# Optimization experiments

Hardware: AMD Instinct MI355X
Metric: run time of the kernel (lower is better)

Reference implementation:

```python
import jax, jax.numpy as jnp
import numpy as np

H = 16
D_NOPE = 128
D_ROPE = 64
D_V = 128
ROPE_BASE = 10000.0
NEG = -1e9


def rotate_half(x):
    h = x.shape[-1] // 2
    return jnp.concatenate([-x[..., h:], x[..., :h]], axis=-1)


def rope_cos_sin(L, dtype=jnp.float32):
    inv_freq = 1.0 / (ROPE_BASE ** (jnp.arange(0, D_ROPE, 2, dtype=jnp.float32) / D_ROPE))
    t = jnp.arange(L, dtype=jnp.float32)
    freqs = jnp.outer(t, inv_freq)                      # (L, D_ROPE/2)
    emb = jnp.concatenate([freqs, freqs], axis=-1)      # (L, D_ROPE)
    return jnp.cos(emb)[None, None].astype(dtype), jnp.sin(emb)[None, None].astype(dtype)


def setup_inputs() -> dict:
    key = jax.random.key(0)
    ks = jax.random.split(key, 8)
    B, L, D = 1, 2048, 2048
    dq, dc = 1536, 512
    dqk = D_NOPE + D_ROPE
    s = 0.02
    hidden_states = jax.random.normal(ks[0], (B, L, D), jnp.float32)
    # causal additive mask, shape (B,1,L,L)
    causal = jnp.tril(jnp.ones((L, L), jnp.bool_))
    attention_mask = jnp.where(causal, 0.0, NEG).astype(jnp.float32)[None, None]
    return {
        "hidden_states": hidden_states,
        "attention_mask": attention_mask,
        "Wq_down": jax.random.normal(ks[1], (D, dq), jnp.float32) * s,
        "Wq_up": jax.random.normal(ks[2], (dq, H * dqk), jnp.float32) * s,
        "Wkv_down": jax.random.normal(ks[3], (D, dc), jnp.float32) * s,
        "Wk_up": jax.random.normal(ks[4], (dc, H * dqk), jnp.float32) * s,
        "Wv_up": jax.random.normal(ks[5], (dc, H * D_V), jnp.float32) * s,
        "Wo": jax.random.normal(ks[6], (H * D_V, D), jnp.float32) * s,
    }


def reference(hidden_states, attention_mask, Wq_down, Wq_up, Wkv_down, Wk_up, Wv_up, Wo):
    B, L, D = hidden_states.shape
    dqk = D_NOPE + D_ROPE
    scale = 1.0 / np.sqrt(dqk).astype(np.float32)

    # low-rank Q path
    q = (hidden_states @ Wq_down) @ Wq_up                       # (B,L,H*dqk)
    q = q.reshape(B, L, H, dqk).transpose(0, 2, 1, 3)           # (B,H,L,dqk)
    # low-rank KV path
    c_kv = hidden_states @ Wkv_down                             # (B,L,dc)
    k = (c_kv @ Wk_up).reshape(B, L, H, dqk).transpose(0, 2, 1, 3)
    v = (c_kv @ Wv_up).reshape(B, L, H, D_V).transpose(0, 2, 1, 3)

    q_nope, q_rope = q[..., :D_NOPE], q[..., D_NOPE:]
    k_nope, k_rope = k[..., :D_NOPE], k[..., D_NOPE:]
    cos, sin = rope_cos_sin(L, hidden_states.dtype)
    q_rope = q_rope * cos + rotate_half(q_rope) * sin
    k_rope = k_rope * cos + rotate_half(k_rope) * sin
    q = jnp.concatenate([q_nope, q_rope], axis=-1)
    k = jnp.concatenate([k_nope, k_rope], axis=-1)

    scores = jnp.einsum("bhqd,bhkd->bhqk", q, k) * scale + attention_mask
    weights = jax.nn.softmax(scores.astype(jnp.float32), axis=-1).astype(q.dtype)
    attn = jnp.einsum("bhqk,bhkd->bhqd", weights, v)            # (B,H,L,D_V)
    attn = attn.transpose(0, 2, 1, 3).reshape(B, L, H * D_V)
    return attn @ Wo
```

## Files before the change

### kernel.cpp

```cpp
#include <hip/hip_runtime.h>
#include <hip/hip_bf16.h>

using bf16 = __hip_bfloat16;
typedef __bf16 bf16x8v __attribute__((ext_vector_type(8)));
typedef float f32x4 __attribute__((ext_vector_type(4)));

static constexpr int SEQ = 2048;
static constexpr int DMODEL = 2048;
static constexpr int NHEADS = 16;
static constexpr int DQKC = 192;
static constexpr int DVC = 128;
static constexpr int DQC = 1536;
static constexpr int DCC = 512;
static constexpr int HQK = NHEADS * DQKC;
static constexpr int HV = NHEADS * DVC;
static constexpr int NKV = HQK + HV;
static constexpr int NDOWN = DQC + DCC;

typedef __attribute__((address_space(1))) const void* gas_ptr;
typedef __attribute__((address_space(3))) void* las_ptr;

__device__ __forceinline__ void g2l16(const void* g, void* l) {
  __builtin_amdgcn_global_load_lds((gas_ptr)g, (las_ptr)l, 16, 0, 0);
}

template <int BM, int BN>
__device__ __forceinline__ void gemm_core(
    const bf16* __restrict__ A, int lda,
    const bf16* __restrict__ Bt, int ldb,
    void* __restrict__ Cv, int ldc,
    int K, float alpha, int c_fp32, long tm, long tn, char* smem)
{
  constexpr int FM = BM / 32, FN = BN / 32;
  bf16* As = (bf16*)smem;
  char* Bsm = smem + BM * 64;
  bf16* Bs = (bf16*)Bsm;
  const int tid = threadIdx.x;
  const int w = tid >> 6, lane = tid & 63;
  const int wm = (w >> 1) * (BM / 2), wn = (w & 1) * (BN / 2);
  const int m0 = lane & 15, q8 = (lane >> 4) * 8;
  f32x4 acc[FM][FN] = {};
  for (int bk = 0; bk < K; bk += 32) {
#pragma unroll
    for (int i = 0; i < BM / 64; i++) {
      const int u = i * 256 + tid;
      g2l16(A + (tm + (u >> 2)) * (long)lda + bk + (u & 3) * 8, smem + u * 16);
    }
#pragma unroll
    for (int i = 0; i < BN / 64; i++) {
      const int u = i * 256 + tid;
      g2l16(Bt + (tn + (u >> 2)) * (long)ldb + bk + (u & 3) * 8, Bsm + u * 16);
    }
    __syncthreads();
    bf16x8v af[FM], bfv[FN];
#pragma unroll
    for (int i = 0; i < FM; i++)
      af[i] = *reinterpret_cast<const bf16x8v*>(&As[(wm + i * 16 + m0) * 32 + q8]);
#pragma unroll
    for (int i = 0; i < FN; i++)
      bfv[i] = *reinterpret_cast<const bf16x8v*>(&Bs[(wn + i * 16 + m0) * 32 + q8]);
#pragma unroll
    for (int mi = 0; mi < FM; mi++)
#pragma unroll
      for (int ni = 0; ni < FN; ni++)
        acc[mi][ni] = __builtin_amdgcn_mfma_f32_16x16x32_bf16(af[mi], bfv[ni], acc[mi][ni], 0, 0, 0);
    __syncthreads();
  }
  const int q4 = (lane >> 4) * 4;
  float* Cf = (float*)Cv;
  bf16* Cb = (bf16*)Cv;
#pragma unroll
  for (int mi = 0; mi < FM; mi++) {
#pragma unroll
    for (int r = 0; r < 4; r++) {
      const long row = tm + wm + mi * 16 + q4 + r;
#pragma unroll
      for (int ni = 0; ni < FN; ni++) {
        const long idx = row * ldc + tn + wn + ni * 16 + m0;
        const float v = acc[mi][ni][r] * alpha;
        if (c_fp32) Cf[idx] = v;
        else Cb[idx] = __float2bfloat16(v);
      }
    }
  }
}

__global__ __launch_bounds__(256) void gemm64(
    const bf16* __restrict__ A, int lda, const bf16* __restrict__ Bt, int ldb,
    void* __restrict__ Cv, int ldc, int K, float alpha, int c_fp32)
{
  __shared__ __align__(16) char smem[(64 + 128) * 64];
  gemm_core<64, 128>(A, lda, Bt, ldb, Cv, ldc, K, alpha, c_fp32,
                     (long)blockIdx.y * 64, (long)blockIdx.x * 128, smem);
}

__global__ __launch_bounds__(256) void gemm_dual(
    const bf16* __restrict__ A1, int lda1, const bf16* __restrict__ B1, int ldb1,
    void* __restrict__ C1, int ldc1, int K1, float alpha1, int nx1,
    const bf16* __restrict__ A2, int lda2, const bf16* __restrict__ B2, int ldb2,
    void* __restrict__ C2, int ldc2, int K2)
{
  __shared__ __align__(16) char smem[(128 + 128) * 64];
  if ((int)blockIdx.x < nx1)
    gemm_core<128, 128>(A1, lda1, B1, ldb1, C1, ldc1, K1, alpha1, 0,
                        (long)blockIdx.y * 128, (long)blockIdx.x * 128, smem);
  else
    gemm_core<128, 128>(A2, lda2, B2, ldb2, C2, ldc2, K2, 1.f, 0,
                        (long)blockIdx.y * 128, (long)((int)blockIdx.x - nx1) * 128, smem);
}

__device__ __forceinline__ void fa_stage(
    const bf16* __restrict__ kvf, const bf16* __restrict__ vT,
    char* smem, int kbase, int vbase, int key0, int h, int tid)
{
#pragma unroll
  for (int i = 0; i < 9; i++) {
    const int u = i * 256 + tid;
    const int key = u / 24;
    const int fg = (u - key * 24) ^ (key & 7);
    g2l16(kvf + (long)(key0 + key) * NKV + h * DQKC + fg * 8, smem + kbase + u * 16);
  }
#pragma unroll
  for (int i = 0; i < 8; i++) {
    const int u = i * 256 + tid;
    const int dv = u >> 4;
    const int kg = (u & 15) ^ (dv & 15);
    g2l16(vT + (long)(h * DVC + dv) * SEQ + key0 + kg * 8, smem + vbase + u * 16);
  }
}

__global__ __launch_bounds__(256) void flash_attn(
    const bf16* __restrict__ qf,
    const bf16* __restrict__ kvf,
    const bf16* __restrict__ vT,
    bf16* __restrict__ attn)
{
  __shared__ __align__(16) char smem[155648];
  const int fid = blockIdx.x;
  const int tile = (fid < 256) ? (31 - (fid >> 4)) : (15 - ((fid - 256) >> 4));
  const int h = fid & 15;
  const int nkt = (tile * 64 + 63) / 96 + 1;
  const int tid = threadIdx.x;
  const int w = tid >> 6, lane = tid & 63;
  const int m0 = lane & 15, quad = lane >> 4;
  const int prow = w * 16 + m0;
  const long qrow = (long)tile * 64 + prow;
  constexpr int PSOFF = 139264;

  bf16x8v qfr[6];
#pragma unroll
  for (int s = 0; s < 6; s++)
    qfr[s] = *reinterpret_cast<const bf16x8v*>(
        &qf[qrow * HQK + h * DQKC + s * 32 + quad * 8]);

  f32x4 O[8] = {};
  float mrow = -1e30f, lrow = 0.f;

  fa_stage(kvf, vT, smem, 0, 73728, 0, h, tid);
  __syncthreads();

  for (int kt = 0; kt < nkt; ++kt) {
    const int cur = kt & 1;
    const int kbase = cur * 36864;
    const int vbase = 73728 + cur * 32768;
    const int key0 = kt * 96;
    if (kt + 1 < nkt)
      fa_stage(kvf, vT, smem, (cur ^ 1) * 36864, 73728 + (cur ^ 1) * 32768,
               key0 + 96, h, tid);

    f32x4 S[6] = {};
#pragma unroll
    for (int s = 0; s < 6; s++) {
#pragma unroll
      for (int mi = 0; mi < 6; mi++) {
        const int kl = mi * 16 + m0;
        const int idx = kl * 24 + ((s * 4 + quad) ^ (m0 & 7));
        const bf16x8v kb = *reinterpret_cast<const bf16x8v*>(smem + kbase + idx * 16);
        S[mi] = __builtin_amdgcn_mfma_f32_16x16x32_bf16(kb, qfr[s], S[mi], 0, 0, 0);
      }
    }
    if (key0 + 95 > tile * 64) {
#pragma unroll
      for (int mi = 0; mi < 6; mi++)
#pragma unroll
        for (int r = 0; r < 4; r++)
          if (key0 + mi * 16 + quad * 4 + r > qrow) S[mi][r] = -1e30f;
    }

    float fm = -1e30f;
#pragma unroll
    for (int mi = 0; mi < 6; mi++)
#pragma unroll
      for (int r = 0; r < 4; r++) fm = fmaxf(fm, S[mi][r]);
    fm = fmaxf(fm, __shfl_xor(fm, 16, 64));
    fm = fmaxf(fm, __shfl_xor(fm, 32, 64));
    const float newm = fmaxf(mrow, fm);
    const float alph = __expf(mrow - newm);
    mrow = newm;
    float ps = 0.f;
#pragma unroll
    for (int mi = 0; mi < 6; mi++)
#pragma unroll
      for (int r = 0; r < 4; r++) {
        const float p = __expf(S[mi][r] - newm);
        S[mi][r] = p;
        ps += p;
      }
    ps += __shfl_xor(ps, 16, 64);
    ps += __shfl_xor(ps, 32, 64);
    lrow = lrow * alph + ps;

#pragma unroll
    for (int mi = 0; mi < 6; mi++) {
      const int k8 = mi * 2 + (quad >> 1);
      const int idx = prow * 16 + (k8 ^ (m0 & 15));
      unsigned short b[4];
#pragma unroll
      for (int r = 0; r < 4; r++) {
        const bf16 t = __float2bfloat16(S[mi][r]);
        b[r] = *reinterpret_cast<const unsigned short*>(&t);
      }
      *reinterpret_cast<uint2*>(smem + PSOFF + idx * 16 + (quad & 1) * 8) =
          make_uint2((unsigned)b[0] | ((unsigned)b[1] << 16),
                     (unsigned)b[2] | ((unsigned)b[3] << 16));
    }
    float aO[4];
#pragma unroll
    for (int r = 0; r < 4; r++) aO[r] = __shfl(alph, quad * 4 + r, 16);
#pragma unroll
    for (int ni = 0; ni < 8; ni++)
#pragma unroll
      for (int r = 0; r < 4; r++) O[ni][r] *= aO[r];

#pragma unroll
    for (int ks = 0; ks < 3; ks++) {
      const int idxp = prow * 16 + ((ks * 4 + quad) ^ (m0 & 15));
      const bf16x8v pa = *reinterpret_cast<const bf16x8v*>(smem + PSOFF + idxp * 16);
#pragma unroll
      for (int ni = 0; ni < 8; ni++) {
        const int dv = ni * 16 + m0;
        const int idxv = dv * 16 + ((ks * 4 + quad) ^ (dv & 15));
        const bf16x8v vb = *reinterpret_cast<const bf16x8v*>(smem + vbase + idxv * 16);
        O[ni] = __builtin_amdgcn_mfma_f32_16x16x32_bf16(pa, vb, O[ni], 0, 0, 0);
      }
    }
    __syncthreads();
  }

  float lO[4];
#pragma unroll
  for (int r = 0; r < 4; r++) lO[r] = 1.f / __shfl(lrow, quad * 4 + r, 16);
#pragma unroll
  for (int ni = 0; ni < 8; ni++)
#pragma unroll
    for (int r = 0; r < 4; r++)
      attn[((long)tile * 64 + w * 16 + quad * 4 + r) * HV + h * DVC + ni * 16 + m0] =
          __float2bfloat16(O[ni][r] * lO[r]);
}

__device__ __forceinline__ float tofl(float x) { return x; }
__device__ __forceinline__ float tofl(bf16 x) { return __bfloat162float(x); }

template <typename TIN>
__global__ __launch_bounds__(256) void transpose_cast(const TIN* __restrict__ in,
                                                      bf16* __restrict__ out,
                                                      int inStride, int outStride) {
  __shared__ float t[32][33];
  const int bx = blockIdx.x * 32, by = blockIdx.y * 32;
  const int tx = threadIdx.x, ty = threadIdx.y;
#pragma unroll
  for (int j = 0; j < 32; j += 8)
    t[ty + j][tx] = tofl(in[(long)(by + ty + j) * inStride + bx + tx]);
  __syncthreads();
#pragma unroll
  for (int j = 0; j < 32; j += 8)
    out[(long)(bx + ty + j) * outStride + by + tx] = __float2bfloat16(t[tx][ty + j]);
}

struct TPar { const float* src; bf16* dst; int C; int R; int gw; int nblk; };

__global__ __launch_bounds__(256) void transpose6(TPar a, TPar b, TPar c,
                                                  TPar d, TPar e, TPar f) {
  int blk = blockIdx.x;
  TPar p;
  if (blk < a.nblk) p = a;
  else { blk -= a.nblk;
  if (blk < b.nblk) p = b;
  else { blk -= b.nblk;
  if (blk < c.nblk) p = c;
  else { blk -= c.nblk;
  if (blk < d.nblk) p = d;
  else { blk -= d.nblk;
  if (blk < e.nblk) p = e;
  else { blk -= e.nblk; p = f; } } } } }
  const int bx = (blk % p.gw) * 32, by = (blk / p.gw) * 32;
  __shared__ float t[32][33];
  const int tx = threadIdx.x, ty = threadIdx.y;
#pragma unroll
  for (int j = 0; j < 32; j += 8)
    t[ty + j][tx] = p.src[(long)(by + ty + j) * p.C + bx + tx];
  __syncthreads();
#pragma unroll
  for (int j = 0; j < 32; j += 8)
    p.dst[(long)(bx + ty + j) * p.R + by + tx] = __float2bfloat16(t[tx][ty + j]);
}

__global__ __launch_bounds__(256) void cast_f32_bf16(const float* __restrict__ in,
                                                     bf16* __restrict__ out, int n4) {
  int i = blockIdx.x * 256 + threadIdx.x;
  if (i < n4) {
    const float4 v = ((const float4*)in)[i];
    out[i * 4 + 0] = __float2bfloat16(v.x);
    out[i * 4 + 1] = __float2bfloat16(v.y);
    out[i * 4 + 2] = __float2bfloat16(v.z);
    out[i * 4 + 3] = __float2bfloat16(v.w);
  }
}

__global__ __launch_bounds__(256) void rope_qk(bf16* __restrict__ q, bf16* __restrict__ k) {
  const int idx = blockIdx.x * 256 + threadIdx.x;
  const int i = idx & 31;
  const int h = (idx >> 5) & 15;
  const int l = idx >> 9;
  const float inv = powf(10000.f, -(float)i * (1.f / 32.f));
  float s, c;
  sincosf((float)l * inv, &s, &c);
  const long qb = (long)l * HQK + h * DQKC + 128;
  const long kb = (long)l * NKV + h * DQKC + 128;
  {
    float x0 = __bfloat162float(q[qb + i]);
    float x1 = __bfloat162float(q[qb + i + 32]);
    q[qb + i] = __float2bfloat16(x0 * c - x1 * s);
    q[qb + i + 32] = __float2bfloat16(x1 * c + x0 * s);
  }
  {
    float x0 = __bfloat162float(k[kb + i]);
    float x1 = __bfloat162float(k[kb + i + 32]);
    k[kb + i] = __float2bfloat16(x0 * c - x1 * s);
    k[kb + i + 32] = __float2bfloat16(x1 * c + x0 * s);
  }
}

extern "C" void kernel_launch(void* const* d_in, const int* in_sizes, int n_in,
                              void* d_out, int out_size, void* d_ws, size_t ws_size,
                              hipStream_t stream) {
  const float* hs      = (const float*)d_in[0];
  const float* Wq_down = (const float*)d_in[2];
  const float* Wq_up   = (const float*)d_in[3];
  const float* Wkv_down= (const float*)d_in[4];
  const float* Wk_up   = (const float*)d_in[5];
  const float* Wv_up   = (const float*)d_in[6];
  const float* Wo      = (const float*)d_in[7];

  char* p = (char*)d_ws;
  auto alloc = [&](long elems) {
    bf16* r = (bf16*)p;
    p += ((elems * 2 + 255) / 256) * 256;
    return r;
  };
  bf16* hsb   = alloc((long)SEQ * DMODEL);
  bf16* W1T   = alloc((long)NDOWN * DMODEL);
  bf16* WquT  = alloc((long)HQK * DQC);
  bf16* WkvuT = alloc((long)NKV * DCC);
  bf16* WoT   = alloc((long)DMODEL * HV);
  bf16* qdc   = alloc((long)SEQ * NDOWN);
  bf16* qf    = alloc((long)SEQ * HQK);
  bf16* kvf   = alloc((long)SEQ * NKV);
  bf16* vT    = alloc((long)HV * SEQ);
  bf16* attn  = alloc((long)SEQ * HV);

  const float scale = 0.07216878364870323f;

  const dim3 b256(256);
  const dim3 tb(32, 8);
  cast_f32_bf16<<<dim3(SEQ * DMODEL / 4 / 256), b256, 0, stream>>>(hs, hsb, SEQ * DMODEL / 4);

  TPar ta{Wq_down,  W1T,                      DQC,    DMODEL, DQC / 32,    (DQC / 32) * (DMODEL / 32)};
  TPar tb2{Wkv_down, W1T + (long)DQC * DMODEL, DCC,    DMODEL, DCC / 32,    (DCC / 32) * (DMODEL / 32)};
  TPar tc{Wq_up,    WquT,                     HQK,    DQC,    HQK / 32,    (HQK / 32) * (DQC / 32)};
  TPar td{Wk_up,    WkvuT,                    HQK,    DCC,    HQK / 32,    (HQK / 32) * (DCC / 32)};
  TPar te{Wv_up,    WkvuT + (long)HQK * DCC,  HV,     DCC,    HV / 32,     (HV / 32) * (DCC / 32)};
  TPar tf{Wo,       WoT,                      DMODEL, HV,     DMODEL / 32, (DMODEL / 32) * (HV / 32)};
  const int tblk = ta.nblk + tb2.nblk + tc.nblk + td.nblk + te.nblk + tf.nblk;
  transpose6<<<dim3(tblk), tb, 0, stream>>>(ta, tb2, tc, td, te, tf);

  gemm64<<<dim3(NDOWN / 128, SEQ / 64), b256, 0, stream>>>(
      hsb, DMODEL, W1T, DMODEL, qdc, NDOWN, DMODEL, 1.f, 0);

  gemm_dual<<<dim3(HQK / 128 + NKV / 128, SEQ / 128), b256, 0, stream>>>(
      qdc, NDOWN, WquT, DQC, qf, HQK, DQC, scale, HQK / 128,
      qdc + DQC, NDOWN, WkvuT, DCC, kvf, NKV, DCC);

  rope_qk<<<dim3(SEQ * NHEADS * 32 / 256), b256, 0, stream>>>(qf, kvf);
  transpose_cast<bf16><<<dim3(HV / 32, SEQ / 32), tb, 0, stream>>>(kvf + HQK, vT, NKV, SEQ);

  flash_attn<<<dim3(512), b256, 0, stream>>>(qf, kvf, vT, attn);

  gemm64<<<dim3(DMODEL / 128, SEQ / 64), b256, 0, stream>>>(
      attn, HV, WoT, HV, d_out, DMODEL, HV, 1.f, 1);
}
```

Before: 338.5 us.

## Split flash attention KV range across two warp groups and enlarge GEMM tiles

Flash attention now launches 512 threads per block, with two 4-wave groups each processing alternating 96-key tiles. Their partial max, sum and output are merged through shared memory at the end. The V tile layout shrinks to 96 keys with a new swizzle, and K/V prefetches are issued after barriers into each group's own buffer. Separately, the down-projection and output GEMMs switch from 64x128 to 128x128 tiles, giving more reuse per block but fewer blocks. The extra barriers and the merge step add overhead.

```diff
diff --git a/kernel.cpp b/kernel.cpp
--- a/kernel.cpp
+++ b/kernel.cpp
@@ -85,13 +85,13 @@
   }
 }
 
-__global__ __launch_bounds__(256) void gemm64(
+__global__ __launch_bounds__(256) void gemm128(
     const bf16* __restrict__ A, int lda, const bf16* __restrict__ Bt, int ldb,
     void* __restrict__ Cv, int ldc, int K, float alpha, int c_fp32)
 {
-  __shared__ __align__(16) char smem[(64 + 128) * 64];
-  gemm_core<64, 128>(A, lda, Bt, ldb, Cv, ldc, K, alpha, c_fp32,
-                     (long)blockIdx.y * 64, (long)blockIdx.x * 128, smem);
+  __shared__ __align__(16) char smem[(128 + 128) * 64];
+  gemm_core<128, 128>(A, lda, Bt, ldb, Cv, ldc, K, alpha, c_fp32,
+                      (long)blockIdx.y * 128, (long)blockIdx.x * 128, smem);
 }
 
 __global__ __launch_bounds__(256) void gemm_dual(
@@ -109,27 +109,32 @@
                         (long)blockIdx.y * 128, (long)((int)blockIdx.x - nx1) * 128, smem);
 }
 
-__device__ __forceinline__ void fa_stage(
-    const bf16* __restrict__ kvf, const bf16* __restrict__ vT,
-    char* smem, int kbase, int vbase, int key0, int h, int tid)
+__device__ __forceinline__ void fa_stage_k(
+    const bf16* __restrict__ kvf, char* smem, int kbase, int key0, int h, int tg)
 {
 #pragma unroll
   for (int i = 0; i < 9; i++) {
-    const int u = i * 256 + tid;
+    const int u = i * 256 + tg;
     const int key = u / 24;
     const int fg = (u - key * 24) ^ (key & 7);
     g2l16(kvf + (long)(key0 + key) * NKV + h * DQKC + fg * 8, smem + kbase + u * 16);
   }
-#pragma unroll
-  for (int i = 0; i < 8; i++) {
-    const int u = i * 256 + tid;
-    const int dv = u >> 4;
-    const int kg = (u & 15) ^ (dv & 15);
-    g2l16(vT + (long)(h * DVC + dv) * SEQ + key0 + kg * 8, smem + vbase + u * 16);
-  }
-}
-
-__global__ __launch_bounds__(256) void flash_attn(
+}
+
+__device__ __forceinline__ void fa_stage_v(
+    const bf16* __restrict__ vT, char* smem, int vbase, int key0, int h, int tg)
+{
+#pragma unroll
+  for (int i = 0; i < 6; i++) {
+    const int u = i * 256 + tg;
+    const int dv = u / 12;
+    const int p = u - dv * 12;
+    const int kgl = p ^ ((dv >> 1) & 3);
+    g2l16(vT + (long)(h * DVC + dv) * SEQ + key0 + kgl * 8, smem + vbase + u * 16);
+  }
+}
+
+__global__ __launch_bounds__(512) void flash_attn(
     const bf16* __restrict__ qf,
     const bf16* __restrict__ kvf,
     const bf16* __restrict__ vT,
@@ -140,12 +145,16 @@
   const int tile = (fid < 256) ? (31 - (fid >> 4)) : (15 - ((fid - 256) >> 4));
   const int h = fid & 15;
   const int nkt = (tile * 64 + 63) / 96 + 1;
+  const int J = (nkt + 1) >> 1;
   const int tid = threadIdx.x;
   const int w = tid >> 6, lane = tid & 63;
+  const int g = w >> 2, wl = w & 3, tg = tid & 255;
   const int m0 = lane & 15, quad = lane >> 4;
-  const int prow = w * 16 + m0;
+  const int prow = wl * 16 + m0;
   const long qrow = (long)tile * 64 + prow;
-  constexpr int PSOFF = 139264;
+  const int kbase = g * 36864;
+  const int vbase = 73728 + g * 24576;
+  const int pbase = 122880 + g * 16384;
 
   bf16x8v qfr[6];
 #pragma unroll
@@ -156,106 +165,145 @@
   f32x4 O[8] = {};
   float mrow = -1e30f, lrow = 0.f;
 
-  fa_stage(kvf, vT, smem, 0, 73728, 0, h, tid);
+  if (g < nkt) {
+    fa_stage_k(kvf, smem, kbase, g * 96, h, tg);
+    fa_stage_v(vT, smem, vbase, g * 96, h, tg);
+  }
   __syncthreads();
 
-  for (int kt = 0; kt < nkt; ++kt) {
-    const int cur = kt & 1;
-    const int kbase = cur * 36864;
-    const int vbase = 73728 + cur * 32768;
+  for (int j = 0; j < J; ++j) {
+    const int kt = 2 * j + g;
+    const bool act = kt < nkt;
     const int key0 = kt * 96;
-    if (kt + 1 < nkt)
-      fa_stage(kvf, vT, smem, (cur ^ 1) * 36864, 73728 + (cur ^ 1) * 32768,
-               key0 + 96, h, tid);
 
     f32x4 S[6] = {};
-#pragma unroll
-    for (int s = 0; s < 6; s++) {
+    if (act) {
+#pragma unroll
+      for (int s = 0; s < 6; s++) {
+#pragma unroll
+        for (int mi = 0; mi < 6; mi++) {
+          const int kl = mi * 16 + m0;
+          const int idx = kl * 24 + ((s * 4 + quad) ^ (m0 & 7));
+          const bf16x8v kb = *reinterpret_cast<const bf16x8v*>(smem + kbase + idx * 16);
+          S[mi] = __builtin_amdgcn_mfma_f32_16x16x32_bf16(kb, qfr[s], S[mi], 0, 0, 0);
+        }
+      }
+    }
+    __syncthreads();
+
+    if (kt + 2 < nkt)
+      fa_stage_k(kvf, smem, kbase, key0 + 192, h, tg);
+
+    if (act) {
+      if (key0 + 95 > tile * 64) {
+#pragma unroll
+        for (int mi = 0; mi < 6; mi++)
+#pragma unroll
+          for (int r = 0; r < 4; r++)
+            if (key0 + mi * 16 + quad * 4 + r > qrow) S[mi][r] = -1e30f;
+      }
+
+      float fm = -1e30f;
+#pragma unroll
+      for (int mi = 0; mi < 6; mi++)
+#pragma unroll
+        for (int r = 0; r < 4; r++) fm = fmaxf(fm, S[mi][r]);
+      fm = fmaxf(fm, __shfl_xor(fm, 16, 64));
+      fm = fmaxf(fm, __shfl_xor(fm, 32, 64));
+      const float newm = fmaxf(mrow, fm);
+      const float alph = __expf(mrow - newm);
+      mrow = newm;
+      float ps = 0.f;
+#pragma unroll
+      for (int mi = 0; mi < 6; mi++)
+#pragma unroll
+        for (int r = 0; r < 4; r++) {
+          const float p = __expf(S[mi][r] - newm);
+          S[mi][r] = p;
+          ps += p;
+        }
+      ps += __shfl_xor(ps, 16, 64);
+      ps += __shfl_xor(ps, 32, 64);
+      lrow = lrow * alph + ps;
+
 #pragma unroll
       for (int mi = 0; mi < 6; mi++) {
-        const int kl = mi * 16 + m0;
-        const int idx = kl * 24 + ((s * 4 + quad) ^ (m0 & 7));
-        const bf16x8v kb = *reinterpret_cast<const bf16x8v*>(smem + kbase + idx * 16);
-        S[mi] = __builtin_amdgcn_mfma_f32_16x16x32_bf16(kb, qfr[s], S[mi], 0, 0, 0);
-      }
-    }
-    if (key0 + 95 > tile * 64) {
-#pragma unroll
-      for (int mi = 0; mi < 6; mi++)
-#pragma unroll
-        for (int r = 0; r < 4; r++)
-          if (key0 + mi * 16 + quad * 4 + r > qrow) S[mi][r] = -1e30f;
-    }
-
-    float fm = -1e30f;
-#pragma unroll
-    for (int mi = 0; mi < 6; mi++)
-#pragma unroll
-      for (int r = 0; r < 4; r++) fm = fmaxf(fm, S[mi][r]);
-    fm = fmaxf(fm, __shfl_xor(fm, 16, 64));
-    fm = fmaxf(fm, __shfl_xor(fm, 32, 64));
-    const float newm = fmaxf(mrow, fm);
-    const float alph = __expf(mrow - newm);
-    mrow = newm;
-    float ps = 0.f;
-#pragma unroll
-    for (int mi = 0; mi < 6; mi++)
+        const int k8 = mi * 2 + (quad >> 1);
+        const int idx = prow * 16 + (k8 ^ (m0 & 15));
+        unsigned short b[4];
+#pragma unroll
+        for (int r = 0; r < 4; r++) {
+          const bf16 t = __float2bfloat16(S[mi][r]);
+          b[r] = *reinterpret_cast<const unsigned short*>(&t);
+        }
+        *reinterpret_cast<uint2*>(smem + pbase + idx * 16 + (quad & 1) * 8) =
+            make_uint2((unsigned)b[0] | ((unsigned)b[1] << 16),
+                       (unsigned)b[2] | ((unsigned)b[3] << 16));
+      }
+      float aO[4];
+#pragma unroll
+      for (int r = 0; r < 4; r++) aO[r] = __shfl(alph, quad * 4 + r, 16);
+#pragma unroll
+      for (int ni = 0; ni < 8; ni++)
+#pragma unroll
+        for (int r = 0; r < 4; r++) O[ni][r] *= aO[r];
+
+#pragma unroll
+      for (int ks = 0; ks < 3; ks++) {
+        const int idxp = prow * 16 + ((ks * 4 + quad) ^ (m0 & 15));
+        const bf16x8v pa = *reinterpret_cast<const bf16x8v*>(smem + pbase + idxp * 16);
+#pragma unroll
+        for (int ni = 0; ni < 8; ni++) {
+          const int dv = ni * 16 + m0;
+          const int idxv = dv * 12 + ((ks * 4 + quad) ^ ((dv >> 1) & 3));
+          const bf16x8v vb = *reinterpret_cast<const bf16x8v*>(smem + vbase + idxv * 16);
+          O[ni] = __builtin_amdgcn_mfma_f32_16x16x32_bf16(pa, vb, O[ni], 0, 0, 0);
+        }
+      }
+    }
+    __syncthreads();
+
+    if (kt + 2 < nkt)
+      fa_stage_v(vT, smem, vbase, key0 + 192, h, tg);
+  }
+
+  float* Om  = (float*)smem;
+  float* Ol  = (float*)(smem + 256);
+  float* O1s = (float*)(smem + 122880);
+  if (g == 1) {
+    if (quad == 0) { Om[prow] = mrow; Ol[prow] = lrow; }
+#pragma unroll
+    for (int ni = 0; ni < 8; ni++)
+#pragma unroll
+      for (int r = 0; r < 4; r++)
+        O1s[(wl * 16 + quad * 4 + r) * 128 + ni * 16 + m0] = O[ni][r];
+  }
+  __syncthreads();
+  if (g == 0) {
+    float a0[4], a1[4];
+#pragma unroll
+    for (int r = 0; r < 4; r++) {
+      const int row = quad * 4 + r;
+      const float m0r = __shfl(mrow, row, 16);
+      const float l0r = __shfl(lrow, row, 16);
+      const float m1r = Om[wl * 16 + row];
+      const float l1r = Ol[wl * 16 + row];
+      const float mm = fmaxf(m0r, m1r);
+      const float e0 = __expf(m0r - mm), e1 = __expf(m1r - mm);
+      const float iv = 1.f / (l0r * e0 + l1r * e1);
+      a0[r] = e0 * iv;
+      a1[r] = e1 * iv;
+    }
+#pragma unroll
+    for (int ni = 0; ni < 8; ni++)
 #pragma unroll
       for (int r = 0; r < 4; r++) {
-        const float p = __expf(S[mi][r] - newm);
-        S[mi][r] = p;
-        ps += p;
-      }
-    ps += __shfl_xor(ps, 16, 64);
-    ps += __shfl_xor(ps, 32, 64);
-    lrow = lrow * alph + ps;
-
-#pragma unroll
-    for (int mi = 0; mi < 6; mi++) {
-      const int k8 = mi * 2 + (quad >> 1);
-      const int idx = prow * 16 + (k8 ^ (m0 & 15));
-      unsigned short b[4];
-#pragma unroll
-      for (int r = 0; r < 4; r++) {
-        const bf16 t = __float2bfloat16(S[mi][r]);
-        b[r] = *reinterpret_cast<const unsigned short*>(&t);
-      }
-      *reinterpret_cast<uint2*>(smem + PSOFF + idx * 16 + (quad & 1) * 8) =
-          make_uint2((unsigned)b[0] | ((unsigned)b[1] << 16),
-                     (unsigned)b[2] | ((unsigned)b[3] << 16));
-    }
-    float aO[4];
-#pragma unroll
-    for (int r = 0; r < 4; r++) aO[r] = __shfl(alph, quad * 4 + r, 16);
-#pragma unroll
-    for (int ni = 0; ni < 8; ni++)
-#pragma unroll
-      for (int r = 0; r < 4; r++) O[ni][r] *= aO[r];
-
-#pragma unroll
-    for (int ks = 0; ks < 3; ks++) {
-      const int idxp = prow * 16 + ((ks * 4 + quad) ^ (m0 & 15));
-      const bf16x8v pa = *reinterpret_cast<const bf16x8v*>(smem + PSOFF + idxp * 16);
-#pragma unroll
-      for (int ni = 0; ni < 8; ni++) {
-        const int dv = ni * 16 + m0;
-        const int idxv = dv * 16 + ((ks * 4 + quad) ^ (dv & 15));
-        const bf16x8v vb = *reinterpret_cast<const bf16x8v*>(smem + vbase + idxv * 16);
-        O[ni] = __builtin_amdgcn_mfma_f32_16x16x32_bf16(pa, vb, O[ni], 0, 0, 0);
-      }
-    }
-    __syncthreads();
-  }
-
-  float lO[4];
-#pragma unroll
-  for (int r = 0; r < 4; r++) lO[r] = 1.f / __shfl(lrow, quad * 4 + r, 16);
-#pragma unroll
-  for (int ni = 0; ni < 8; ni++)
-#pragma unroll
-    for (int r = 0; r < 4; r++)
-      attn[((long)tile * 64 + w * 16 + quad * 4 + r) * HV + h * DVC + ni * 16 + m0] =
-          __float2bfloat16(O[ni][r] * lO[r]);
+        const float v = O[ni][r] * a0[r] +
+                        O1s[(wl * 16 + quad * 4 + r) * 128 + ni * 16 + m0] * a1[r];
+        attn[((long)tile * 64 + wl * 16 + quad * 4 + r) * HV + h * DVC + ni * 16 + m0] =
+            __float2bfloat16(v);
+      }
+  }
 }
 
 __device__ __forceinline__ float tofl(float x) { return x; }
@@ -384,7 +432,7 @@
   const int tblk = ta.nblk + tb2.nblk + tc.nblk + td.nblk + te.nblk + tf.nblk;
   transpose6<<<dim3(tblk), tb, 0, stream>>>(ta, tb2, tc, td, te, tf);
 
-  gemm64<<<dim3(NDOWN / 128, SEQ / 64), b256, 0, stream>>>(
+  gemm128<<<dim3(NDOWN / 128, SEQ / 128), b256, 0, stream>>>(
       hsb, DMODEL, W1T, DMODEL, qdc, NDOWN, DMODEL, 1.f, 0);
 
   gemm_dual<<<dim3(HQK / 128 + NKV / 128, SEQ / 128), b256, 0, stream>>>(
@@ -394,8 +442,8 @@
   rope_qk<<<dim3(SEQ * NHEADS * 32 / 256), b256, 0, stream>>>(qf, kvf);
   transpose_cast<bf16><<<dim3(HV / 32, SEQ / 32), tb, 0, stream>>>(kvf + HQK, vT, NKV, SEQ);
 
-  flash_attn<<<dim3(512), b256, 0, stream>>>(qf, kvf, vT, attn);
-
-  gemm64<<<dim3(DMODEL / 128, SEQ / 64), b256, 0, stream>>>(
+  flash_attn<<<dim3(512), dim3(512), 0, stream>>>(qf, kvf, vT, attn);
+
+  gemm128<<<dim3(DMODEL / 128, SEQ / 128), b256, 0, stream>>>(
       attn, HV, WoT, HV, d_out, DMODEL, HV, 1.f, 1);
 }
```

Measured after the change: 344.7 us. No clear change (+1.8%).
